# Optimization experiments

Measured on AMD Instinct MI355X. Metric: run time of the kernel, lower is better.

The kernel has to match this reference:

```python
import jax, jax.numpy as jnp
import numpy as np

EMBED_DIM = 1024
NUM_HEADS = 16
HEAD_DIM = EMBED_DIM // NUM_HEADS


def setup_inputs() -> dict:
    key = jax.random.key(0)
    ks = jax.random.split(key, 9)
    s = 1.0 / np.sqrt(EMBED_DIM)
    x = jax.random.normal(ks[0], (4, 2048, EMBED_DIM), dtype=jnp.float32)
    # torch.nn.Linear weights are [out_features, in_features]
    Wq = jax.random.uniform(ks[1], (EMBED_DIM, EMBED_DIM), jnp.float32, -s, s)
    bq = jax.random.uniform(ks[2], (EMBED_DIM,), jnp.float32, -s, s)
    Wk = jax.random.uniform(ks[3], (EMBED_DIM, EMBED_DIM), jnp.float32, -s, s)
    bk = jax.random.uniform(ks[4], (EMBED_DIM,), jnp.float32, -s, s)
    Wv = jax.random.uniform(ks[5], (EMBED_DIM, EMBED_DIM), jnp.float32, -s, s)
    bv = jax.random.uniform(ks[6], (EMBED_DIM,), jnp.float32, -s, s)
    Wo = jax.random.uniform(ks[7], (EMBED_DIM, EMBED_DIM), jnp.float32, -s, s)
    bo = jax.random.uniform(ks[8], (EMBED_DIM,), jnp.float32, -s, s)
    return {"x": x, "Wq": Wq, "bq": bq, "Wk": Wk, "bk": bk,
            "Wv": Wv, "bv": bv, "Wo": Wo, "bo": bo}


def reference(x, Wq, bq, Wk, bk, Wv, bv, Wo, bo):
    B, S, E = x.shape
    H, D = NUM_HEADS, HEAD_DIM

    def proj(W, b):
        y = jnp.einsum('bse,fe->bsf', x, W) + b          # Linear: x @ W.T + b
        return y.reshape(B, S, H, D).transpose(0, 2, 1, 3)  # [B,H,S,D]

    q = proj(Wq, bq)
    k = proj(Wk, bk)
    v = proj(Wv, bv)

    scores = jnp.einsum('bhqd,bhkd->bhqk', q, k) / jnp.sqrt(jnp.float32(D))
    attn = jax.nn.soft_sign(scores)                      # softsign, no normalization
    # dropout p=0.0 -> identity
    ctx = jnp.einsum('bhqk,bhkd->bhqd', attn, v)         # [B,H,S,D]
    ctx = ctx.transpose(0, 2, 1, 3).reshape(B, S, E)
    out = jnp.einsum('bse,fe->bsf', ctx, Wo) + bo
    return (out,)
```

## Files before the change

kernel.cpp:

```cpp
#include <hip/hip_runtime.h>
#include <hip/hip_bf16.h>
#include <stdint.h>

#define Bb 4
#define SEQ 2048
#define Ee 1024
#define Hh 16
#define Dh 64
#define Mm (Bb*SEQ)

typedef __attribute__((ext_vector_type(8))) short bfrag;
typedef __attribute__((ext_vector_type(4))) float f32x4;
typedef __attribute__((ext_vector_type(16))) float f32x16;
typedef unsigned short u16;

__device__ __forceinline__ u16 f2bf(float x) {
  __hip_bfloat16 h = __float2bfloat16(x);
  return *reinterpret_cast<u16*>(&h);
}

__device__ __forceinline__ void gll16(const void* g, void* l) {
  __builtin_amdgcn_global_load_lds(
      (const __attribute__((address_space(1))) void*)g,
      (__attribute__((address_space(3))) void*)l, 16, 0, 0);
}

__global__ __launch_bounds__(256) void cast_all(
    const float* __restrict__ x,  const float* __restrict__ wq,
    const float* __restrict__ wk, const float* __restrict__ wv,
    const float* __restrict__ wo,
    u16* __restrict__ xb, u16* __restrict__ wqb, u16* __restrict__ wkb,
    u16* __restrict__ wvb, u16* __restrict__ wob)
{
  int idx = blockIdx.x * 256 + threadIdx.x;
  const float* src; u16* dst; int off;
  if (idx < 2097152) { src = x; dst = xb; off = idx; }
  else {
    int t = idx - 2097152;
    int seg = t >> 18;
    off = t & 262143;
    src = (seg == 0) ? wq : (seg == 1) ? wk : (seg == 2) ? wv : wo;
    dst = (seg == 0) ? wqb : (seg == 1) ? wkb : (seg == 2) ? wvb : wob;
  }
  float4 v = reinterpret_cast<const float4*>(src)[off];
  ushort4 o;
  o.x = f2bf(v.x); o.y = f2bf(v.y); o.z = f2bf(v.z); o.w = f2bf(v.w);
  reinterpret_cast<ushort4*>(dst)[off] = o;
}

template<int OUTMODE>
__global__ __launch_bounds__(256) void gemm_bt(
    const u16* __restrict__ A,
    const u16* __restrict__ W0, const u16* __restrict__ W1, const u16* __restrict__ W2,
    const float* __restrict__ b0, const float* __restrict__ b1, const float* __restrict__ b2,
    void* __restrict__ outp, int K, int N)
{
  __shared__ __align__(16) u16 smem[16384];
  u16* As = smem;
  u16* Bs = smem + 8192;
  const int tid  = threadIdx.x;
  const int lane = tid & 63;
  const int wid  = tid >> 6;
  const int bm = blockIdx.x * 128;
  const int bn = blockIdx.y * 128;
  const int z  = blockIdx.z;
  const u16*  Wp = (z == 0) ? W0 : (z == 1) ? W1 : W2;
  const float* bp = (z == 0) ? b0 : (z == 1) ? b1 : b2;
  const int wr = (wid >> 1) * 64, wc = (wid & 1) * 64;
  const int lr = lane & 15, lk = (lane >> 4) * 8;
  f32x4 acc[4][4] = {};

  for (int kt = 0; kt < K; kt += 64) {
    __syncthreads();
#pragma unroll
    for (int p = 0; p < 4; ++p) {
      int flat = p * 2048 + tid * 8;
      int r = flat >> 6, c = flat & 63;
      gll16(A + (size_t)(bm + r) * K + kt + c, As + flat);
    }
#pragma unroll
    for (int p = 0; p < 4; ++p) {
      int flat = p * 2048 + tid * 8;
      int r = flat >> 6, c = flat & 63;
      gll16(Wp + (size_t)(bn + r) * K + kt + c, Bs + flat);
    }
    __syncthreads();
#pragma unroll
    for (int kk = 0; kk < 2; ++kk) {
      bfrag a[4], b[4];
#pragma unroll
      for (int i = 0; i < 4; ++i)
        a[i] = *reinterpret_cast<const bfrag*>(&As[(wr + i * 16 + lr) * 64 + kk * 32 + lk]);
#pragma unroll
      for (int j = 0; j < 4; ++j)
        b[j] = *reinterpret_cast<const bfrag*>(&Bs[(wc + j * 16 + lr) * 64 + kk * 32 + lk]);
#pragma unroll
      for (int i = 0; i < 4; ++i)
#pragma unroll
        for (int j = 0; j < 4; ++j)
          acc[i][j] = __builtin_amdgcn_mfma_f32_16x16x32_bf16(a[i], b[j], acc[i][j], 0, 0, 0);
    }
  }

  float bias[4];
#pragma unroll
  for (int j = 0; j < 4; ++j) bias[j] = bp[bn + wc + j * 16 + (lane & 15)];

  if (OUTMODE == 0) {
    __syncthreads();
    u16* cst = smem;
#pragma unroll
    for (int i = 0; i < 4; ++i)
#pragma unroll
      for (int j = 0; j < 4; ++j)
#pragma unroll
        for (int e = 0; e < 4; ++e)
          cst[(wr + i * 16 + (lane >> 4) * 4 + e) * 128 + wc + j * 16 + (lane & 15)] =
              f2bf(acc[i][j][e] + bias[j]);
    __syncthreads();
    u16* outb = (u16*)outp + (size_t)z * (size_t)Mm * Ee;
#pragma unroll
    for (int p = 0; p < 8; ++p) {
      int chunk = p * 256 + tid;
      int r = chunk >> 4;
      int c = (chunk & 15) * 8;
      int m = bm + r, f = bn + c;
      u16* dst = outb + ((((size_t)(m >> 11) * Hh + (f >> 6)) * SEQ + (m & 2047)) * Dh + (f & 63));
      *reinterpret_cast<bfrag*>(dst) = *reinterpret_cast<const bfrag*>(&cst[r * 128 + c]);
    }
  } else {
    float* outf = (float*)outp;
    float* cf = reinterpret_cast<float*>(smem);
#pragma unroll
    for (int half = 0; half < 2; ++half) {
      __syncthreads();
      if ((wid >> 1) == half) {
#pragma unroll
        for (int i = 0; i < 4; ++i)
#pragma unroll
          for (int j = 0; j < 4; ++j)
#pragma unroll
            for (int e = 0; e < 4; ++e)
              cf[(i * 16 + (lane >> 4) * 4 + e) * 128 + wc + j * 16 + (lane & 15)] =
                  acc[i][j][e] + bias[j];
      }
      __syncthreads();
#pragma unroll
      for (int p = 0; p < 8; ++p) {
        int chunk = p * 256 + tid;
        int r = chunk >> 5;
        int c = (chunk & 31) * 4;
        *reinterpret_cast<float4*>(&outf[(size_t)(bm + half * 64 + r) * N + bn + c]) =
            *reinterpret_cast<const float4*>(&cf[r * 128 + c]);
      }
    }
  }
}

__global__ __launch_bounds__(256) void transpose_v(const u16* __restrict__ v,
                                                   u16* __restrict__ vt)
{
  __shared__ __align__(16) u16 lds[8192];
  const int tid = threadIdx.x;
  const int bh = blockIdx.y;
  const int st = blockIdx.x * 128;
  const u16* vb = v + (size_t)bh * SEQ * Dh;
#pragma unroll
  for (int p = 0; p < 4; ++p) {
    int flat = p * 2048 + tid * 8;
    int s = flat >> 6, dp = flat & 63;
    int dl = dp ^ (((s >> 3) & 7) << 3);
    gll16(vb + (size_t)(st + s) * Dh + dl, lds + flat);
  }
  __syncthreads();
  u16* vtb = vt + (size_t)bh * Dh * SEQ;
#pragma unroll
  for (int p = 0; p < 4; ++p) {
    int chunk = p * 256 + tid;
    int sc = chunk & 15, d = chunk >> 4;
    bfrag o;
#pragma unroll
    for (int e = 0; e < 8; ++e) {
      int sp = sc * 8 + e;
      int ss = (sp & 0x63) | ((sp & 4) << 1) | ((sp & 8) >> 1) | (sp & 0x70);
      ss = (sp & ~12) | ((sp & 4) << 1) | ((sp & 8) >> 1);
      int X = ((ss >> 3) & 7) << 3;
      o[e] = (short)lds[ss * 64 + (d ^ X)];
    }
    *reinterpret_cast<bfrag*>(&vtb[(size_t)d * SEQ + st + sc * 8]) = o;
  }
}

__global__ __launch_bounds__(256) void attn_kernel(
    const u16* __restrict__ qg_, const u16* __restrict__ kg,
    const u16* __restrict__ vtg, u16* __restrict__ ctx)
{
  __shared__ __align__(16) u16 smem[16384];
  const int tid  = threadIdx.x;
  const int lane = tid & 63;
  const int wid  = tid >> 6;
  const int ql = lane & 31;
  const int hi = lane >> 5;

  const int orig = blockIdx.x;
  const int swz  = (orig & 7) * 64 + (orig >> 3);
  const int bh = swz >> 3;
  const int q0 = (swz & 7) * 256;

  const u16* qb  = qg_ + (size_t)bh * SEQ * Dh;
  const u16* kb  = kg  + (size_t)bh * SEQ * Dh;
  const u16* vtb = vtg + (size_t)bh * Dh * SEQ;

  bfrag qf[2][4];
#pragma unroll
  for (int qg2 = 0; qg2 < 2; ++qg2)
#pragma unroll
    for (int db = 0; db < 4; ++db)
      qf[qg2][db] = *reinterpret_cast<const bfrag*>(
          &qb[(size_t)(q0 + wid * 64 + qg2 * 32 + ql) * Dh + db * 16 + hi * 8]);

  f32x16 o[2][2] = {};

  auto stage = [&](int kt, int buf) {
#pragma unroll
    for (int p = 0; p < 2; ++p) {
      int flat = p * 2048 + tid * 8;
      int r = flat >> 6, cp = flat & 63;
      int cl = cp ^ ((r & 7) << 3);
      gll16(kb + (size_t)(kt + r) * Dh + cl, smem + buf * 4096 + flat);
    }
#pragma unroll
    for (int p = 0; p < 2; ++p) {
      int flat = p * 2048 + tid * 8;
      int r = flat >> 6, cp = flat & 63;
      int cl = cp ^ ((r & 7) << 3);
      gll16(vtb + (size_t)r * SEQ + kt + cl, smem + 8192 + buf * 4096 + flat);
    }
  };

  stage(0, 0);
  __syncthreads();

  for (int ti = 0; ti < 32; ++ti) {
    const int cur = ti & 1;
    if (ti < 31) stage((ti + 1) * 64, cur ^ 1);
    const u16* Kb = smem + cur * 4096;
    const u16* Vb = smem + 8192 + cur * 4096;

#pragma unroll
    for (int kh = 0; kh < 2; ++kh) {
      f32x16 s[2] = {};
      const int krow = kh * 32 + ql;
      const int ksw = (krow & 7) << 3;
#pragma unroll
      for (int db = 0; db < 4; ++db) {
        bfrag ka = *reinterpret_cast<const bfrag*>(
            &Kb[krow * 64 + ((db * 16 + hi * 8) ^ ksw)]);
        s[0] = __builtin_amdgcn_mfma_f32_32x32x16_bf16(ka, qf[0][db], s[0], 0, 0, 0);
        s[1] = __builtin_amdgcn_mfma_f32_32x32x16_bf16(ka, qf[1][db], s[1], 0, 0, 0);
      }
      bfrag pa[2][2];
#pragma unroll
      for (int qg2 = 0; qg2 < 2; ++qg2)
#pragma unroll
        for (int r = 0; r < 16; ++r) {
          float sv = s[qg2][r];
          float pv = sv * __builtin_amdgcn_rcpf(8.0f + __builtin_fabsf(sv));
          pa[qg2][r >> 3][r & 7] = (short)f2bf(pv);
        }
#pragma unroll
      for (int tt = 0; tt < 2; ++tt)
#pragma unroll
        for (int dh = 0; dh < 2; ++dh) {
          const int vrow = dh * 32 + ql;
          bfrag vb = *reinterpret_cast<const bfrag*>(
              &Vb[vrow * 64 + ((kh * 32 + tt * 16 + hi * 8) ^ ((vrow & 7) << 3))]);
          o[0][dh] = __builtin_amdgcn_mfma_f32_32x32x16_bf16(pa[0][tt], vb, o[0][dh], 0, 0, 0);
          o[1][dh] = __builtin_amdgcn_mfma_f32_32x32x16_bf16(pa[1][tt], vb, o[1][dh], 0, 0, 0);
        }
    }
    __syncthreads();
  }

  u16* cst = smem;
#pragma unroll
  for (int qg2 = 0; qg2 < 2; ++qg2)
#pragma unroll
    for (int dh = 0; dh < 2; ++dh)
#pragma unroll
      for (int r = 0; r < 16; ++r) {
        int qrow = wid * 64 + qg2 * 32 + (r & 3) + 8 * (r >> 2) + 4 * hi;
        cst[qrow * 64 + dh * 32 + ql] = f2bf(o[qg2][dh][r]);
      }
  __syncthreads();
  const int b = bh >> 4, h = bh & 15;
#pragma unroll
  for (int p = 0; p < 8; ++p) {
    int chunk = p * 256 + tid;
    int r = chunk >> 3, cc = (chunk & 7) * 8;
    u16* dst = ctx + ((size_t)(b * SEQ + q0 + r) * Ee + h * Dh + cc);
    *reinterpret_cast<bfrag*>(dst) = *reinterpret_cast<const bfrag*>(&cst[r * 64 + cc]);
  }
}

extern "C" void kernel_launch(void* const* d_in, const int* in_sizes, int n_in,
                              void* d_out, int out_size, void* d_ws, size_t ws_size,
                              hipStream_t stream)
{
  const float* x  = (const float*)d_in[0];
  const float* Wq = (const float*)d_in[1];
  const float* bq = (const float*)d_in[2];
  const float* Wk = (const float*)d_in[3];
  const float* bk = (const float*)d_in[4];
  const float* Wv = (const float*)d_in[5];
  const float* bv = (const float*)d_in[6];
  const float* Wo = (const float*)d_in[7];
  const float* bo = (const float*)d_in[8];
  float* out = (float*)d_out;

  u16* ws  = (u16*)d_ws;
  u16* xb  = ws;
  u16* wqb = ws + 8388608;
  u16* wkb = wqb + 1048576;
  u16* wvb = wkb + 1048576;
  u16* wob = wvb + 1048576;
  u16* qkv = wob + 1048576;
  u16* q_  = qkv;
  u16* k_  = qkv + 8388608;
  u16* v_  = qkv + 2 * 8388608;
  u16* vt  = xb;
  u16* ctx = v_;

  cast_all<<<12288, 256, 0, stream>>>(x, Wq, Wk, Wv, Wo, xb, wqb, wkb, wvb, wob);

  gemm_bt<0><<<dim3(64, 8, 3), 256, 0, stream>>>(xb, wqb, wkb, wvb, bq, bk, bv,
                                                 qkv, Ee, Ee);
  transpose_v<<<dim3(16, 64), 256, 0, stream>>>(v_, vt);
  attn_kernel<<<512, 256, 0, stream>>>(q_, k_, vt, ctx);
  gemm_bt<1><<<dim3(64, 8, 1), 256, 0, stream>>>(ctx, wob, wob, wob, bo, bo, bo,
                                                 out, Ee, Ee);
}
```

Baseline: 305.4 us.

## Shrink attention query tile, fold scale into Q, retune LDS swizzle and occupancy

The attention kernel now handles 128 queries per block (32 per wave) instead of 256, doubling the grid to 1024 blocks and requesting 4 blocks per CU through launch bounds. The 1/sqrt(D) scale is folded into the Q projection epilogue, so softsign becomes s/(1+|s|). The bf16 packing now truncates two floats at a time with a byte perm instead of rounding each one. K/V LDS staging uses a 128-wide swizzle with precomputed offsets, and MFMA sections are wrapped in setprio. The aim is more occupancy and less per-element VALU work, at the cost of less Q reuse per K/V tile loaded and truncation instead of round-to-nearest.

```diff
diff --git a/kernel.cpp b/kernel.cpp
--- a/kernel.cpp
+++ b/kernel.cpp
@@ -12,6 +12,7 @@
 typedef __attribute__((ext_vector_type(8))) short bfrag;
 typedef __attribute__((ext_vector_type(4))) float f32x4;
 typedef __attribute__((ext_vector_type(16))) float f32x16;
+typedef __attribute__((ext_vector_type(4))) unsigned u32x4;
 typedef unsigned short u16;
 
 __device__ __forceinline__ u16 f2bf(float x) {
@@ -107,6 +108,7 @@
   for (int j = 0; j < 4; ++j) bias[j] = bp[bn + wc + j * 16 + (lane & 15)];
 
   if (OUTMODE == 0) {
+    const float scl = (z == 0) ? 0.125f : 1.0f;
     __syncthreads();
     u16* cst = smem;
 #pragma unroll
@@ -116,7 +118,7 @@
 #pragma unroll
         for (int e = 0; e < 4; ++e)
           cst[(wr + i * 16 + (lane >> 4) * 4 + e) * 128 + wc + j * 16 + (lane & 15)] =
-              f2bf(acc[i][j][e] + bias[j]);
+              f2bf((acc[i][j][e] + bias[j]) * scl);
     __syncthreads();
     u16* outb = (u16*)outp + (size_t)z * (size_t)Mm * Ee;
 #pragma unroll
@@ -182,8 +184,7 @@
 #pragma unroll
     for (int e = 0; e < 8; ++e) {
       int sp = sc * 8 + e;
-      int ss = (sp & 0x63) | ((sp & 4) << 1) | ((sp & 8) >> 1) | (sp & 0x70);
-      ss = (sp & ~12) | ((sp & 4) << 1) | ((sp & 8) >> 1);
+      int ss = (sp & ~12) | ((sp & 4) << 1) | ((sp & 8) >> 1);
       int X = ((ss >> 3) & 7) << 3;
       o[e] = (short)lds[ss * 64 + (d ^ X)];
     }
@@ -191,7 +192,7 @@
   }
 }
 
-__global__ __launch_bounds__(256) void attn_kernel(
+__global__ __launch_bounds__(256, 4) void attn_kernel(
     const u16* __restrict__ qg_, const u16* __restrict__ kg,
     const u16* __restrict__ vtg, u16* __restrict__ ctx)
 {
@@ -203,39 +204,41 @@
   const int hi = lane >> 5;
 
   const int orig = blockIdx.x;
-  const int swz  = (orig & 7) * 64 + (orig >> 3);
-  const int bh = swz >> 3;
-  const int q0 = (swz & 7) * 256;
+  const int swz  = (orig & 7) * 128 + (orig >> 3);
+  const int bh = swz >> 4;
+  const int q0 = (swz & 15) * 128;
 
   const u16* qb  = qg_ + (size_t)bh * SEQ * Dh;
   const u16* kb  = kg  + (size_t)bh * SEQ * Dh;
   const u16* vtb = vtg + (size_t)bh * Dh * SEQ;
 
-  bfrag qf[2][4];
-#pragma unroll
-  for (int qg2 = 0; qg2 < 2; ++qg2)
-#pragma unroll
-    for (int db = 0; db < 4; ++db)
-      qf[qg2][db] = *reinterpret_cast<const bfrag*>(
-          &qb[(size_t)(q0 + wid * 64 + qg2 * 32 + ql) * Dh + db * 16 + hi * 8]);
-
-  f32x16 o[2][2] = {};
+  bfrag qf[4];
+#pragma unroll
+  for (int db = 0; db < 4; ++db)
+    qf[db] = *reinterpret_cast<const bfrag*>(
+        &qb[(size_t)(q0 + wid * 32 + ql) * Dh + db * 16 + hi * 8]);
+
+  int koff[2], voff[2];
+#pragma unroll
+  for (int p = 0; p < 2; ++p) {
+    int f = p * 2048 + tid * 8;
+    int lrow = f >> 7;
+    int log7 = (f & 127) ^ ((lrow & 15) << 3);
+    int r = lrow * 2 + (log7 >> 6);
+    int c = log7 & 63;
+    koff[p] = r * 64 + c;
+    voff[p] = r * SEQ + c;
+  }
+
+  f32x16 o[2] = {};
 
   auto stage = [&](int kt, int buf) {
 #pragma unroll
-    for (int p = 0; p < 2; ++p) {
-      int flat = p * 2048 + tid * 8;
-      int r = flat >> 6, cp = flat & 63;
-      int cl = cp ^ ((r & 7) << 3);
-      gll16(kb + (size_t)(kt + r) * Dh + cl, smem + buf * 4096 + flat);
-    }
-#pragma unroll
-    for (int p = 0; p < 2; ++p) {
-      int flat = p * 2048 + tid * 8;
-      int r = flat >> 6, cp = flat & 63;
-      int cl = cp ^ ((r & 7) << 3);
-      gll16(vtb + (size_t)r * SEQ + kt + cl, smem + 8192 + buf * 4096 + flat);
-    }
+    for (int p = 0; p < 2; ++p)
+      gll16(kb + (size_t)kt * 64 + koff[p], smem + buf * 4096 + p * 2048 + tid * 8);
+#pragma unroll
+    for (int p = 0; p < 2; ++p)
+      gll16(vtb + kt + voff[p], smem + 8192 + buf * 4096 + p * 2048 + tid * 8);
   };
 
   stage(0, 0);
@@ -249,53 +252,63 @@
 
 #pragma unroll
     for (int kh = 0; kh < 2; ++kh) {
-      f32x16 s[2] = {};
-      const int krow = kh * 32 + ql;
-      const int ksw = (krow & 7) << 3;
+      f32x16 s = {};
+      __builtin_amdgcn_s_setprio(1);
 #pragma unroll
       for (int db = 0; db < 4; ++db) {
+        const int krow = kh * 32 + ql;
+        const int lr2 = krow >> 1;
+        const int log7 = ((krow & 1) << 6) | (db * 16 + hi * 8);
         bfrag ka = *reinterpret_cast<const bfrag*>(
-            &Kb[krow * 64 + ((db * 16 + hi * 8) ^ ksw)]);
-        s[0] = __builtin_amdgcn_mfma_f32_32x32x16_bf16(ka, qf[0][db], s[0], 0, 0, 0);
-        s[1] = __builtin_amdgcn_mfma_f32_32x32x16_bf16(ka, qf[1][db], s[1], 0, 0, 0);
+            &Kb[lr2 * 128 + (log7 ^ ((lr2 & 15) << 3))]);
+        s = __builtin_amdgcn_mfma_f32_32x32x16_bf16(ka, qf[db], s, 0, 0, 0);
       }
-      bfrag pa[2][2];
-#pragma unroll
-      for (int qg2 = 0; qg2 < 2; ++qg2)
-#pragma unroll
-        for (int r = 0; r < 16; ++r) {
-          float sv = s[qg2][r];
-          float pv = sv * __builtin_amdgcn_rcpf(8.0f + __builtin_fabsf(sv));
-          pa[qg2][r >> 3][r & 7] = (short)f2bf(pv);
-        }
+      __builtin_amdgcn_s_setprio(0);
+
+      unsigned pw[8];
+#pragma unroll
+      for (int r = 0; r < 8; ++r) {
+        float a = s[2 * r], b = s[2 * r + 1];
+        float pa_ = a * __builtin_amdgcn_rcpf(1.0f + __builtin_fabsf(a));
+        float pb_ = b * __builtin_amdgcn_rcpf(1.0f + __builtin_fabsf(b));
+        pw[r] = __builtin_amdgcn_perm(__builtin_bit_cast(unsigned, pb_),
+                                      __builtin_bit_cast(unsigned, pa_),
+                                      0x07060302u);
+      }
+      u32x4 w0 = {pw[0], pw[1], pw[2], pw[3]};
+      u32x4 w1 = {pw[4], pw[5], pw[6], pw[7]};
+      bfrag pa0 = __builtin_bit_cast(bfrag, w0);
+      bfrag pa1 = __builtin_bit_cast(bfrag, w1);
+
+      __builtin_amdgcn_s_setprio(1);
 #pragma unroll
       for (int tt = 0; tt < 2; ++tt)
 #pragma unroll
         for (int dh = 0; dh < 2; ++dh) {
           const int vrow = dh * 32 + ql;
+          const int lr2 = vrow >> 1;
+          const int log7 = ((vrow & 1) << 6) | (kh * 32 + tt * 16 + hi * 8);
           bfrag vb = *reinterpret_cast<const bfrag*>(
-              &Vb[vrow * 64 + ((kh * 32 + tt * 16 + hi * 8) ^ ((vrow & 7) << 3))]);
-          o[0][dh] = __builtin_amdgcn_mfma_f32_32x32x16_bf16(pa[0][tt], vb, o[0][dh], 0, 0, 0);
-          o[1][dh] = __builtin_amdgcn_mfma_f32_32x32x16_bf16(pa[1][tt], vb, o[1][dh], 0, 0, 0);
+              &Vb[lr2 * 128 + (log7 ^ ((lr2 & 15) << 3))]);
+          o[dh] = __builtin_amdgcn_mfma_f32_32x32x16_bf16(tt ? pa1 : pa0, vb, o[dh], 0, 0, 0);
         }
+      __builtin_amdgcn_s_setprio(0);
     }
     __syncthreads();
   }
 
   u16* cst = smem;
 #pragma unroll
-  for (int qg2 = 0; qg2 < 2; ++qg2)
-#pragma unroll
-    for (int dh = 0; dh < 2; ++dh)
-#pragma unroll
-      for (int r = 0; r < 16; ++r) {
-        int qrow = wid * 64 + qg2 * 32 + (r & 3) + 8 * (r >> 2) + 4 * hi;
-        cst[qrow * 64 + dh * 32 + ql] = f2bf(o[qg2][dh][r]);
-      }
+  for (int dh = 0; dh < 2; ++dh)
+#pragma unroll
+    for (int r = 0; r < 16; ++r) {
+      int qrow = wid * 32 + (r & 3) + 8 * (r >> 2) + 4 * hi;
+      cst[qrow * 64 + dh * 32 + ql] = f2bf(o[dh][r]);
+    }
   __syncthreads();
   const int b = bh >> 4, h = bh & 15;
 #pragma unroll
-  for (int p = 0; p < 8; ++p) {
+  for (int p = 0; p < 4; ++p) {
     int chunk = p * 256 + tid;
     int r = chunk >> 3, cc = (chunk & 7) * 8;
     u16* dst = ctx + ((size_t)(b * SEQ + q0 + r) * Ee + h * Dh + cc);
@@ -336,7 +349,7 @@
   gemm_bt<0><<<dim3(64, 8, 3), 256, 0, stream>>>(xb, wqb, wkb, wvb, bq, bk, bv,
                                                  qkv, Ee, Ee);
   transpose_v<<<dim3(16, 64), 256, 0, stream>>>(v_, vt);
-  attn_kernel<<<512, 256, 0, stream>>>(q_, k_, vt, ctx);
+  attn_kernel<<<1024, 256, 0, stream>>>(q_, k_, vt, ctx);
   gemm_bt<1><<<dim3(64, 8, 1), 256, 0, stream>>>(ctx, wob, wob, wob, bo, bo, bo,
                                                  out, Ee, Ee);
 }
```

Result: no change. 299.4 us (-1.9%).
